# Performance work log

Measured on AMD Instinct MI355X. Metric: run time of the kernel, lower is better.

## Reference

```python
import jax, jax.numpy as jnp
import numpy as np

N, E, F_IN, H, EF, G, GFD = 50000, 800000, 64, 128, 8, 10, 2
NEG_SLOPE = 0.2  # PyG GATv2Conv default negative_slope


def _gatv2_layer(x, src, dst, edge_attr, Wl, bl, Wr, br, We, att, bias):
    # PyG GATv2Conv, heads=1, concat=True, share_weights=False
    n = x.shape[0]
    xl = x @ Wl + bl            # source transform [N,H]
    xr = x @ Wr + br            # target transform [N,H]
    e = edge_attr @ We          # edge embedding   [E,H]
    s = jax.nn.leaky_relu(xl[src] + xr[dst] + e, NEG_SLOPE)  # [E,H]
    logits = s @ att            # [E]
    # numerically-stable segment softmax over destination nodes
    mx = jax.ops.segment_max(logits, dst, num_segments=n)
    mx = jnp.where(jnp.isfinite(mx), mx, 0.0)
    ex = jnp.exp(logits - mx[dst])
    den = jax.ops.segment_sum(ex, dst, num_segments=n)
    alpha = ex / jnp.maximum(den[dst], 1e-16)
    out = jax.ops.segment_sum(alpha[:, None] * xl[src], dst, num_segments=n)
    return out + bias


def _forward(x, edge_index, edge_attr, graph_features, num_graphs, params, head_W, head_b):
    src, dst = edge_index[0], edge_index[1]
    for (Wl, bl, Wr, br, We, att, bias) in params:
        x = jax.nn.relu(_gatv2_layer(x, src, dst, edge_attr, Wl, bl, Wr, br, We, att, bias))
        # dropout p=0.0 / eval mode: no-op
    n_nodes = x.shape[0] // num_graphs
    # faithful replication of the torch reshape chain (graph_feature_dim == 2):
    # graph_features.T [GFD,G] -> unsqueeze(2) -> repeat to [GFD,G,Np] -> view(G,GFD,Np)
    # -> cat(unbind(0), dim=1) -> [GFD, G*Np]
    gf = jnp.broadcast_to(graph_features.T[:, :, None], (GFD, num_graphs, n_nodes))
    gf = gf.reshape(num_graphs, GFD, n_nodes)
    gf = gf.transpose(1, 0, 2).reshape(GFD, num_graphs * n_nodes)
    x = jnp.concatenate([x, gf.T], axis=1)  # [N, H+GFD]
    return x @ head_W + head_b


def setup_inputs():
    key = jax.random.key(0)
    ks = list(jax.random.split(key, 32))
    p = lambda k, s: jax.random.normal(k, s, jnp.float32) * 0.05
    inp = {
        'x': jax.random.normal(ks[0], (N, F_IN), jnp.float32),
        'edge_index': jax.random.randint(ks[1], (2, E), 0, N),
        'edge_attr': jax.random.normal(ks[2], (E, EF), jnp.float32),
        'graph_features': jax.random.normal(ks[3], (G, GFD), jnp.float32),
        'num_graphs': G,
    }
    i = 4
    for l in range(3):
        fin = F_IN if l == 0 else H
        inp[f'Wl{l}'] = p(ks[i], (fin, H)); i += 1
        inp[f'bl{l}'] = jnp.zeros((H,), jnp.float32)
        inp[f'Wr{l}'] = p(ks[i], (fin, H)); i += 1
        inp[f'br{l}'] = jnp.zeros((H,), jnp.float32)
        inp[f'We{l}'] = p(ks[i], (EF, H)); i += 1
        inp[f'att{l}'] = p(ks[i], (H,)); i += 1
        inp[f'bias{l}'] = jnp.zeros((H,), jnp.float32)
    inp['head_W'] = p(ks[i], (H + GFD, 1))
    inp['head_b'] = jnp.zeros((1,), jnp.float32)
    return inp


def reference(x, edge_index, edge_attr, graph_features, num_graphs,
              Wl0, bl0, Wr0, br0, We0, att0, bias0,
              Wl1, bl1, Wr1, br1, We1, att1, bias1,
              Wl2, bl2, Wr2, br2, We2, att2, bias2,
              head_W, head_b):
    params = [(Wl0, bl0, Wr0, br0, We0, att0, bias0),
              (Wl1, bl1, Wr1, br1, We1, att1, bias1),
              (Wl2, bl2, Wr2, br2, We2, att2, bias2)]
    return _forward(x, edge_index, edge_attr, graph_features, num_graphs, params, head_W, head_b)
```

## Files before the change

kernel.cpp:

```cpp
#include <hip/hip_runtime.h>
#include <hip/hip_bf16.h>
#include <math.h>

#define NN 50000
#define EE 800000
#define F_IN 64
#define HH 128
#define EF 8
#define GG 10
#define GFD 2
#define NEG_SLOPE 0.2f
#define NB 64

typedef float v2f __attribute__((ext_vector_type(2)));
__device__ __forceinline__ v2f fma2(v2f a, v2f b, v2f c) {
  return __builtin_elementwise_fma(a, b, c);
}
__device__ __forceinline__ v2f bc2(float x) { v2f r; r.x = x; r.y = x; return r; }

template <int CTRL>
__device__ __forceinline__ float dpp_add(float v) {
  int p = __builtin_amdgcn_update_dpp(0, __float_as_int(v), CTRL, 0xf, 0xf, true);
  return v + __int_as_float(p);
}
__device__ __forceinline__ float red32(float v) {
  v = dpp_add<0xB1>(v);
  v = dpp_add<0x4E>(v);
  v = dpp_add<0x141>(v);
  v = dpp_add<0x140>(v);
  v += __int_as_float(__builtin_amdgcn_ds_swizzle(__float_as_int(v), 0x401F));
  return v;
}

__device__ __forceinline__ void lin2_body(
    int bid, const float* __restrict__ x, int fin,
    const float* __restrict__ Wl, const float* __restrict__ bl,
    const float* __restrict__ Wr, const float* __restrict__ br,
    float* __restrict__ xl, float* __restrict__ xr, int n_nodes) {
  __shared__ float xs[64 * 128];
  const int tid = threadIdx.x;
  const int base = bid * 64;
  int nrows = n_nodes - base; if (nrows > 64) nrows = 64;

  const int total4 = (nrows * fin) >> 2;
  const float4* xsrc = (const float4*)(x + (size_t)base * fin);
  float4* xd = (float4*)xs;
  for (int i = tid; i < total4; i += 256) xd[i] = xsrc[i];
  __syncthreads();

  const int lane = tid & 63;
  const int w = tid >> 6;
  const int c = lane * 2;

  float accl0[16], accl1[16], accr0[16], accr1[16];
#pragma unroll
  for (int j = 0; j < 16; j++) { accl0[j]=0.f; accl1[j]=0.f; accr0[j]=0.f; accr1[j]=0.f; }

  const float* xrow = xs + (w * 16) * fin;
  for (int k = 0; k < fin; k += 4) {
    float2 wl0 = *(const float2*)(Wl + (size_t)k * HH + c);
    float2 wl1 = *(const float2*)(Wl + (size_t)(k + 1) * HH + c);
    float2 wl2 = *(const float2*)(Wl + (size_t)(k + 2) * HH + c);
    float2 wl3 = *(const float2*)(Wl + (size_t)(k + 3) * HH + c);
    float2 wr0 = *(const float2*)(Wr + (size_t)k * HH + c);
    float2 wr1 = *(const float2*)(Wr + (size_t)(k + 1) * HH + c);
    float2 wr2 = *(const float2*)(Wr + (size_t)(k + 2) * HH + c);
    float2 wr3 = *(const float2*)(Wr + (size_t)(k + 3) * HH + c);
#pragma unroll
    for (int j = 0; j < 16; j++) {
      float4 xv = *(const float4*)(xrow + j * fin + k);
      accl0[j] = fmaf(xv.x, wl0.x, accl0[j]);
      accl1[j] = fmaf(xv.x, wl0.y, accl1[j]);
      accr0[j] = fmaf(xv.x, wr0.x, accr0[j]);
      accr1[j] = fmaf(xv.x, wr0.y, accr1[j]);
      accl0[j] = fmaf(xv.y, wl1.x, accl0[j]);
      accl1[j] = fmaf(xv.y, wl1.y, accl1[j]);
      accr0[j] = fmaf(xv.y, wr1.x, accr0[j]);
      accr1[j] = fmaf(xv.y, wr1.y, accr1[j]);
      accl0[j] = fmaf(xv.z, wl2.x, accl0[j]);
      accl1[j] = fmaf(xv.z, wl2.y, accl1[j]);
      accr0[j] = fmaf(xv.z, wr2.x, accr0[j]);
      accr1[j] = fmaf(xv.z, wr2.y, accr1[j]);
      accl0[j] = fmaf(xv.w, wl3.x, accl0[j]);
      accl1[j] = fmaf(xv.w, wl3.y, accl1[j]);
      accr0[j] = fmaf(xv.w, wr3.x, accr0[j]);
      accr1[j] = fmaf(xv.w, wr3.y, accr1[j]);
    }
  }
  float2 blv = *(const float2*)(bl + c);
  float2 brv = *(const float2*)(br + c);
#pragma unroll
  for (int j = 0; j < 16; j++) {
    int n = base + w * 16 + j;
    if (n < n_nodes) {
      *(float2*)(xl + (size_t)n * HH + c) = make_float2(accl0[j] + blv.x, accl1[j] + blv.y);
      *(float2*)(xr + (size_t)n * HH + c) = make_float2(accr0[j] + brv.x, accr1[j] + brv.y);
    }
  }
}

__global__ __launch_bounds__(256) void lin2_kernel(
    const float* __restrict__ x, int fin,
    const float* __restrict__ Wl, const float* __restrict__ bl,
    const float* __restrict__ Wr, const float* __restrict__ br,
    float* __restrict__ xl, float* __restrict__ xr, int n_nodes) {
  lin2_body(blockIdx.x, x, fin, Wl, bl, Wr, br, xl, xr, n_nodes);
}

__device__ __forceinline__ void hist_body(int bid, const int* __restrict__ dst,
                                          int* __restrict__ hist, int ne) {
  int i = bid * 256 + threadIdx.x;
  if (i < ne) atomicAdd(&hist[dst[i]], 1);
}

__global__ __launch_bounds__(256) void fusedA_kernel(
    int nl2, const float* __restrict__ x, int fin,
    const float* __restrict__ Wl, const float* __restrict__ bl,
    const float* __restrict__ Wr, const float* __restrict__ br,
    float* __restrict__ xl, float* __restrict__ xr, int n_nodes,
    const int* __restrict__ dst, int* __restrict__ hist, int ne) {
  if ((int)blockIdx.x < nl2)
    lin2_body(blockIdx.x, x, fin, Wl, bl, Wr, br, xl, xr, n_nodes);
  else
    hist_body(blockIdx.x - nl2, dst, hist, ne);
}

__global__ __launch_bounds__(1024) void reduce_kernel(const int* __restrict__ hist,
                                                      int* __restrict__ bsum, int n) {
  __shared__ int wsum[16];
  const int tid = threadIdx.x;
  const int lane = tid & 63, w = tid >> 6;
  int i = blockIdx.x * 1024 + tid;
  int v = (i < n) ? hist[i] : 0;
#pragma unroll
  for (int off = 32; off; off >>= 1) v += __shfl_xor(v, off);
  if (lane == 0) wsum[w] = v;
  __syncthreads();
  if (tid < 16) {
    int s = wsum[tid];
#pragma unroll
    for (int off = 8; off; off >>= 1) s += __shfl_xor(s, off);
    if (tid == 0) bsum[blockIdx.x] = s;
  }
}

__global__ __launch_bounds__(64) void scanb_kernel(const int* __restrict__ bsum,
                                                   int* __restrict__ bbase,
                                                   int* __restrict__ offs, int nb, int n) {
  const int tid = threadIdx.x;
  int v = (tid < nb) ? bsum[tid] : 0;
  int inc = v;
#pragma unroll
  for (int d = 1; d < 64; d <<= 1) {
    int t2 = __shfl_up(inc, d);
    if (tid >= d) inc += t2;
  }
  if (tid < nb) bbase[tid] = inc - v;
  if (tid == 63) offs[n] = inc;
}

__global__ __launch_bounds__(1024) void scanc_kernel(const int* __restrict__ hist,
                                                     const int* __restrict__ bbase,
                                                     int* __restrict__ offs,
                                                     int* __restrict__ cursor, int n) {
  __shared__ int wsum[16], wpre[16];
  const int tid = threadIdx.x;
  const int lane = tid & 63, w = tid >> 6;
  int i = blockIdx.x * 1024 + tid;
  int orig = (i < n) ? hist[i] : 0;
  int v = orig;
#pragma unroll
  for (int d = 1; d < 64; d <<= 1) {
    int t2 = __shfl_up(v, d);
    if (lane >= d) v += t2;
  }
  if (lane == 63) wsum[w] = v;
  __syncthreads();
  if (tid < 16) {
    int s = wsum[tid];
    int inc = s;
#pragma unroll
    for (int d = 1; d < 16; d <<= 1) {
      int t2 = __shfl_up(inc, d);
      if (tid >= d) inc += t2;
    }
    wpre[tid] = inc - s;
  }
  __syncthreads();
  if (i < n) {
    int ex = bbase[blockIdx.x] + wpre[w] + (v - orig);
    offs[i] = ex; cursor[i] = ex;
  }
}

__device__ __forceinline__ void scatter_body(
    int bid, const int* __restrict__ src, const int* __restrict__ dst,
    int* __restrict__ cursor, int* __restrict__ pk,
    const float4* __restrict__ ea4, float4* __restrict__ eas, int ne) {
  int i = bid * 256 + threadIdx.x;
  if (i < ne) {
    int d = dst[i];
    int pos = atomicAdd(&cursor[d], 1);
    pk[pos] = src[i] * 512;
    float4 a = ea4[i * 2], b = ea4[i * 2 + 1];
    eas[pos * 2] = a; eas[pos * 2 + 1] = b;
  }
}

__device__ __forceinline__ void deg_hist_body(int bid, const int* __restrict__ offs,
                                              int* __restrict__ hist2, int n) {
  __shared__ int lhist[NB];
  const int tid = threadIdx.x;
  int i = bid * 256 + tid;
  if (tid < NB) lhist[tid] = 0;
  __syncthreads();
  if (i < n) {
    int d = offs[i + 1] - offs[i];
    int key = NB - 1 - min(d, NB - 1);
    atomicAdd(&lhist[key], 1);
  }
  __syncthreads();
  if (tid < NB && lhist[tid]) atomicAdd(&hist2[tid], lhist[tid]);
}

__global__ __launch_bounds__(256) void fusedB_kernel(
    int nsc, const int* __restrict__ src, const int* __restrict__ dst,
    int* __restrict__ cursor, int* __restrict__ pk,
    const float4* __restrict__ ea4, float4* __restrict__ eas, int ne,
    const int* __restrict__ offs, int* __restrict__ hist2, int n) {
  if ((int)blockIdx.x < nsc)
    scatter_body(blockIdx.x, src, dst, cursor, pk, ea4, eas, ne);
  else
    deg_hist_body(blockIdx.x - nsc, offs, hist2, n);
}

__global__ __launch_bounds__(64) void scan64_kernel(const int* __restrict__ hist2,
                                                    int* __restrict__ cursor2) {
  const int tid = threadIdx.x;
  int v = hist2[tid];
  int inc = v;
#pragma unroll
  for (int d = 1; d < 64; d <<= 1) {
    int t2 = __shfl_up(inc, d);
    if (tid >= d) inc += t2;
  }
  cursor2[tid] = inc - v;
}

__global__ __launch_bounds__(256) void deg_scatter_kernel(const int* __restrict__ offs,
                                                          int* __restrict__ cursor2,
                                                          int4* __restrict__ meta4, int n) {
  __shared__ int lhist[NB];
  __shared__ int lbase[NB];
  const int tid = threadIdx.x;
  int i = blockIdx.x * 256 + tid;
  if (tid < NB) lhist[tid] = 0;
  __syncthreads();
  int key = 0, rank = 0, bb = 0, ee = 0;
  const bool valid = (i < n);
  if (valid) {
    bb = offs[i]; ee = offs[i + 1];
    int d = ee - bb;
    key = NB - 1 - min(d, NB - 1);
    rank = atomicAdd(&lhist[key], 1);
  }
  __syncthreads();
  if (tid < NB && lhist[tid]) lbase[tid] = atomicAdd(&cursor2[tid], lhist[tid]);
  __syncthreads();
  if (valid) meta4[lbase[key] + rank] = make_int4(bb, ee, i, 0);
}

__global__ __launch_bounds__(256, 4) void gat_fused_kernel(
    const float* __restrict__ xl, const float* __restrict__ xr,
    const float* __restrict__ eas, const float* __restrict__ We,
    const float* __restrict__ att,
    const int* __restrict__ pk, const int4* __restrict__ meta4,
    const float* __restrict__ bias,
    float* __restrict__ xout, int n_nodes,
    float* __restrict__ out_head, const float* __restrict__ hw,
    const float* __restrict__ hb) {
  const int lane = threadIdx.x & 63;
  const int g = lane >> 5, t = lane & 31;
  const int c = t * 4;
  const int tb = t * 16;
  const int nwaves = gridDim.x * 4;

  v2f wea[EF], web[EF];
#pragma unroll
  for (int k = 0; k < EF; k++) {
    float4 w4 = *(const float4*)(We + k * HH + c);
    wea[k].x = w4.x; wea[k].y = w4.y;
    web[k].x = w4.z; web[k].y = w4.w;
  }
  const float4 at = *(const float4*)(att + c);
  const float4 bi = *(const float4*)(bias + c);
  const char* xlb = (const char*)xl;
  const char* easb = (const char*)eas;
  float4 hwv = make_float4(0.f, 0.f, 0.f, 0.f);
  float hw0 = 0.f, hw1 = 0.f, hb0 = 0.f;
  if (out_head) {
    hwv = *(const float4*)(hw + c);
    hw0 = hw[HH]; hw1 = hw[HH + 1]; hb0 = hb[0];
  }

  int wid = blockIdx.x * 4 + (threadIdx.x >> 6);
  if (wid >= n_nodes) return;
  int4 mt = meta4[wid];
  float4 vr4 = *(const float4*)(xr + (size_t)mt.z * HH + c);

  while (true) {
    const int b = mt.x, e = mt.y, node = mt.z;
    const int deg = e - b;
    const int nwid = wid + nwaves;
    const bool hasN = nwid < n_nodes;
    int4 mtN = mt;
    if (hasN) mtN = meta4[nwid];

    v2f vra; vra.x = vr4.x; vra.y = vr4.y;
    v2f vrb; vrb.x = vr4.z; vrb.y = vr4.w;

    float4 o;
    if (deg == 0) {
      o.x = fmaxf(bi.x, 0.f); o.y = fmaxf(bi.y, 0.f);
      o.z = fmaxf(bi.z, 0.f); o.w = fmaxf(bi.w, 0.f);
    } else {
      const int emax = e - 1;
      v2f acc0 = bc2(0.f), acc1 = bc2(0.f);
      float den = 0.f;
      v2f vlAa, vlAb, epA0, epA1, eqA0, eqA1;
      v2f vlBa, vlBb, epB0, epB1, eqB0, eqB1;

#define LOADS(VLa, VLb, P0, P1, Q0, Q1, IDX)                        \
  do {                                                              \
    int _cx = min((IDX), emax);                                     \
    float4 _ep = *(const float4*)(easb + (_cx << 5));               \
    float4 _eq = *(const float4*)(easb + (_cx << 5) + 16);          \
    int _ob = pk[_cx];                                              \
    float4 _vl = *(const float4*)(xlb + (_ob + tb));                \
    P0.x = _ep.x; P0.y = _ep.y; P1.x = _ep.z; P1.y = _ep.w;         \
    Q0.x = _eq.x; Q0.y = _eq.y; Q1.x = _eq.z; Q1.y = _eq.w;         \
    VLa.x = _vl.x; VLa.y = _vl.y; VLb.x = _vl.z; VLb.y = _vl.w;     \
  } while (0)

#define PROCESS(VLa, VLb, P0, P1, Q0, Q1, IDX)                       \
  do {                                                               \
    v2f s0 = VLa + vra;                                              \
    v2f s1 = VLb + vrb;                                              \
    s0 = fma2(bc2(P0.x), wea[0], s0); s1 = fma2(bc2(P0.x), web[0], s1); \
    s0 = fma2(bc2(P0.y), wea[1], s0); s1 = fma2(bc2(P0.y), web[1], s1); \
    s0 = fma2(bc2(P1.x), wea[2], s0); s1 = fma2(bc2(P1.x), web[2], s1); \
    s0 = fma2(bc2(P1.y), wea[3], s0); s1 = fma2(bc2(P1.y), web[3], s1); \
    s0 = fma2(bc2(Q0.x), wea[4], s0); s1 = fma2(bc2(Q0.x), web[4], s1); \
    s0 = fma2(bc2(Q0.y), wea[5], s0); s1 = fma2(bc2(Q0.y), web[5], s1); \
    s0 = fma2(bc2(Q1.x), wea[6], s0); s1 = fma2(bc2(Q1.x), web[6], s1); \
    s0 = fma2(bc2(Q1.y), wea[7], s0); s1 = fma2(bc2(Q1.y), web[7], s1); \
    v2f m0 = s0 * bc2(NEG_SLOPE);                                    \
    v2f m1 = s1 * bc2(NEG_SLOPE);                                    \
    float l0 = fmaxf(s0.x, m0.x), l1 = fmaxf(s0.y, m0.y);            \
    float l2 = fmaxf(s1.x, m1.x), l3 = fmaxf(s1.y, m1.y);            \
    float v = l0 * at.x;                                             \
    v = fmaf(l1, at.y, v);                                           \
    v = fmaf(l2, at.z, v);                                           \
    v = fmaf(l3, at.w, v);                                           \
    v = red32(v);                                                    \
    const float p = ((IDX) < e) ? __expf(v) : 0.f;                   \
    den += p;                                                        \
    acc0 = fma2(bc2(p), VLa, acc0);                                  \
    acc1 = fma2(bc2(p), VLb, acc1);                                  \
  } while (0)

      int idx = b + g;
      LOADS(vlAa, vlAb, epA0, epA1, eqA0, eqA1, idx);
      LOADS(vlBa, vlBb, epB0, epB1, eqB0, eqB1, idx + 2);

      const int nit = (deg + 3) >> 2;
      for (int j = 0; j < nit; j++) {
        PROCESS(vlAa, vlAb, epA0, epA1, eqA0, eqA1, idx);
        LOADS(vlAa, vlAb, epA0, epA1, eqA0, eqA1, idx + 4);
        PROCESS(vlBa, vlBb, epB0, epB1, eqB0, eqB1, idx + 2);
        LOADS(vlBa, vlBb, epB0, epB1, eqB0, eqB1, idx + 6);
        idx += 4;
      }
#undef LOADS
#undef PROCESS

      den += __shfl_xor(den, 32);
      float a0 = acc0.x + __shfl_xor(acc0.x, 32);
      float a1 = acc0.y + __shfl_xor(acc0.y, 32);
      float a2 = acc1.x + __shfl_xor(acc1.x, 32);
      float a3 = acc1.y + __shfl_xor(acc1.y, 32);

      const float inv = 1.f / fmaxf(den, 1e-16f);
      o.x = fmaxf(fmaf(a0, inv, bi.x), 0.f);
      o.y = fmaxf(fmaf(a1, inv, bi.y), 0.f);
      o.z = fmaxf(fmaf(a2, inv, bi.z), 0.f);
      o.w = fmaxf(fmaf(a3, inv, bi.w), 0.f);
    }

    float4 vrN = vr4;
    if (hasN) vrN = *(const float4*)(xr + (size_t)mtN.z * HH + c);

    if (!out_head) {
      if (g == 0) *(float4*)(xout + (size_t)node * HH + c) = o;
    } else {
      float hv = o.x * hwv.x + o.y * hwv.y + o.z * hwv.z + o.w * hwv.w;
      hv = red32(hv);
      if (lane == 0) {
        int k = node / (NN / GG);
        int i0 = 2 * k, i1 = 2 * k + 1;
        float gf0 = xout[(i0 % GG) * GFD + (i0 / GG)];
        float gf1 = xout[(i1 % GG) * GFD + (i1 / GG)];
        out_head[node] = hv + gf0 * hw0 + gf1 * hw1 + hb0;
      }
    }

    if (!hasN) break;
    wid = nwid; mt = mtN; vr4 = vrN;
  }
}

extern "C" void kernel_launch(void* const* d_in, const int* in_sizes, int n_in,
                              void* d_out, int out_size, void* d_ws, size_t ws_size,
                              hipStream_t stream) {
  const float* x_in = (const float*)d_in[0];
  const int*   eidx = (const int*)d_in[1];
  const float* ea   = (const float*)d_in[2];
  const float* gf   = (const float*)d_in[3];
  const int* src = eidx;
  const int* dst = eidx + EE;
  const float* head_W = (const float*)d_in[26];
  const float* head_b = (const float*)d_in[27];
  float* out = (float*)d_out;

  const int NCHUNK = (NN + 1023) / 1024;
  const int NL2B = (NN + 63) / 64;
  const int NHB  = (EE + 255) / 256;
  const int NDB  = (NN + 255) / 256;

  float* P      = (float*)d_ws;
  float* Q      = P + (size_t)NN * HH;
  float* R      = Q + (size_t)NN * HH;
  float* eas    = R + (size_t)NN * HH;
  int*   pk     = (int*)(eas + (size_t)EE * EF);
  int*   hist   = pk + EE;
  int*   hist2  = hist + NN;
  int*   offs   = hist2 + NB;
  int*   cursor = offs + NN + 1;
  int*   cursor2= cursor + NN;
  int*   bsum   = cursor2 + NB;
  int*   bbase  = bsum + NCHUNK;
  int4*  meta4  = (int4*)(((size_t)(bbase + NCHUNK) + 15) & ~(size_t)15);

  const float* Wl0 = (const float*)d_in[5], *bl0 = (const float*)d_in[6];
  const float* Wr0 = (const float*)d_in[7], *br0 = (const float*)d_in[8];

  (void)hipMemsetAsync(hist, 0, (NN + NB) * sizeof(int), stream);
  fusedA_kernel<<<NL2B + NHB, 256, 0, stream>>>(NL2B, x_in, F_IN, Wl0, bl0, Wr0, br0,
                                                P, Q, NN, dst, hist, EE);
  reduce_kernel<<<NCHUNK, 1024, 0, stream>>>(hist, bsum, NN);
  scanb_kernel<<<1, 64, 0, stream>>>(bsum, bbase, offs, NCHUNK, NN);
  scanc_kernel<<<NCHUNK, 1024, 0, stream>>>(hist, bbase, offs, cursor, NN);
  fusedB_kernel<<<NHB + NDB, 256, 0, stream>>>(NHB, src, dst, cursor, pk,
                                               (const float4*)ea, (float4*)eas, EE,
                                               offs, hist2, NN);
  scan64_kernel<<<1, 64, 0, stream>>>(hist2, cursor2);
  deg_scatter_kernel<<<NDB, 256, 0, stream>>>(offs, cursor2, meta4, NN);

  for (int l = 0; l < 3; l++) {
    const float* We   = (const float*)d_in[5 + 7 * l + 4];
    const float* att  = (const float*)d_in[5 + 7 * l + 5];
    const float* bias = (const float*)d_in[5 + 7 * l + 6];

    if (l > 0) {
      const float* Wl = (const float*)d_in[5 + 7 * l + 0];
      const float* bl = (const float*)d_in[5 + 7 * l + 1];
      const float* Wr = (const float*)d_in[5 + 7 * l + 2];
      const float* br = (const float*)d_in[5 + 7 * l + 3];
      lin2_kernel<<<NL2B, 256, 0, stream>>>(R, HH, Wl, bl, Wr, br, P, Q, NN);
    }
    if (l < 2) {
      gat_fused_kernel<<<2048, 256, 0, stream>>>(P, Q, eas, We, att, pk, meta4,
                                                 bias, R, NN, nullptr, nullptr, nullptr);
    } else {
      gat_fused_kernel<<<2048, 256, 0, stream>>>(P, Q, eas, We, att, pk, meta4,
                                                 bias, (float*)gf, NN, out, head_W, head_b);
    }
  }
}
```

Before: 482.1 us.

## Merge scan kernels with grid barrier and split edge-attr scatter into gather pass

Replaces the three-kernel reduce/scan-base/scan-chunk sequence with a single kernel that publishes per-chunk sums and spins on an atomic counter before computing each chunk's base. The CSR scatter now writes only a packed (src offset, edge byte offset) pair. A separate gather pass, fused with the degree-scatter kernel, then reads the edge attributes into sorted order, so the random writes become random reads. This trims kernel launches and makes the scatter writes smaller, but relies on all 49 chunk blocks being co-resident for the spin barrier. It also adds an extra pass over the pair array.

After: 501.6 us. 4.0% more time.

```diff
diff --git a/kernel.cpp b/kernel.cpp
--- a/kernel.cpp
+++ b/kernel.cpp
@@ -125,48 +125,15 @@
     hist_body(blockIdx.x - nl2, dst, hist, ne);
 }
 
-__global__ __launch_bounds__(1024) void reduce_kernel(const int* __restrict__ hist,
-                                                      int* __restrict__ bsum, int n) {
-  __shared__ int wsum[16];
+__global__ __launch_bounds__(1024) void scan_all_kernel(
+    const int* __restrict__ hist, int* __restrict__ offs, int* __restrict__ cursor,
+    int* __restrict__ bsum, int* __restrict__ done, int n, int nchunk) {
+  __shared__ int wsum[16], wpre[16];
+  __shared__ int chtot_s, base_s;
   const int tid = threadIdx.x;
   const int lane = tid & 63, w = tid >> 6;
-  int i = blockIdx.x * 1024 + tid;
-  int v = (i < n) ? hist[i] : 0;
-#pragma unroll
-  for (int off = 32; off; off >>= 1) v += __shfl_xor(v, off);
-  if (lane == 0) wsum[w] = v;
-  __syncthreads();
-  if (tid < 16) {
-    int s = wsum[tid];
-#pragma unroll
-    for (int off = 8; off; off >>= 1) s += __shfl_xor(s, off);
-    if (tid == 0) bsum[blockIdx.x] = s;
-  }
-}
-
-__global__ __launch_bounds__(64) void scanb_kernel(const int* __restrict__ bsum,
-                                                   int* __restrict__ bbase,
-                                                   int* __restrict__ offs, int nb, int n) {
-  const int tid = threadIdx.x;
-  int v = (tid < nb) ? bsum[tid] : 0;
-  int inc = v;
-#pragma unroll
-  for (int d = 1; d < 64; d <<= 1) {
-    int t2 = __shfl_up(inc, d);
-    if (tid >= d) inc += t2;
-  }
-  if (tid < nb) bbase[tid] = inc - v;
-  if (tid == 63) offs[n] = inc;
-}
-
-__global__ __launch_bounds__(1024) void scanc_kernel(const int* __restrict__ hist,
-                                                     const int* __restrict__ bbase,
-                                                     int* __restrict__ offs,
-                                                     int* __restrict__ cursor, int n) {
-  __shared__ int wsum[16], wpre[16];
-  const int tid = threadIdx.x;
-  const int lane = tid & 63, w = tid >> 6;
-  int i = blockIdx.x * 1024 + tid;
+  const int bid = blockIdx.x;
+  int i = bid * 1024 + tid;
   int orig = (i < n) ? hist[i] : 0;
   int v = orig;
 #pragma unroll
@@ -185,25 +152,42 @@
       if (tid >= d) inc += t2;
     }
     wpre[tid] = inc - s;
+    if (tid == 15) chtot_s = inc;
+  }
+  __syncthreads();
+  if (tid == 0) {
+    bsum[bid] = chtot_s;
+    __threadfence();
+    atomicAdd(done, 1);
+    while (atomicAdd(done, 0) < nchunk) __builtin_amdgcn_s_sleep(8);
+  }
+  __syncthreads();
+  if (tid < 64) {
+    int bv = (tid < nchunk) ? atomicAdd(&bsum[tid], 0) : 0;
+    int inc = bv;
+#pragma unroll
+    for (int d = 1; d < 64; d <<= 1) {
+      int t2 = __shfl_up(inc, d);
+      if (tid >= d) inc += t2;
+    }
+    if (tid == bid) base_s = inc - bv;
+    if (bid == nchunk - 1 && tid == nchunk - 1) offs[n] = inc;
   }
   __syncthreads();
   if (i < n) {
-    int ex = bbase[blockIdx.x] + wpre[w] + (v - orig);
+    int ex = base_s + wpre[w] + (v - orig);
     offs[i] = ex; cursor[i] = ex;
   }
 }
 
 __device__ __forceinline__ void scatter_body(
     int bid, const int* __restrict__ src, const int* __restrict__ dst,
-    int* __restrict__ cursor, int* __restrict__ pk,
-    const float4* __restrict__ ea4, float4* __restrict__ eas, int ne) {
+    int* __restrict__ cursor, int2* __restrict__ pk2, int ne) {
   int i = bid * 256 + threadIdx.x;
   if (i < ne) {
     int d = dst[i];
     int pos = atomicAdd(&cursor[d], 1);
-    pk[pos] = src[i] * 512;
-    float4 a = ea4[i * 2], b = ea4[i * 2 + 1];
-    eas[pos * 2] = a; eas[pos * 2 + 1] = b;
+    pk2[pos] = make_int2(src[i] * 512, i * 32);
   }
 }
 
@@ -225,11 +209,10 @@
 
 __global__ __launch_bounds__(256) void fusedB_kernel(
     int nsc, const int* __restrict__ src, const int* __restrict__ dst,
-    int* __restrict__ cursor, int* __restrict__ pk,
-    const float4* __restrict__ ea4, float4* __restrict__ eas, int ne,
+    int* __restrict__ cursor, int2* __restrict__ pk2, int ne,
     const int* __restrict__ offs, int* __restrict__ hist2, int n) {
   if ((int)blockIdx.x < nsc)
-    scatter_body(blockIdx.x, src, dst, cursor, pk, ea4, eas, ne);
+    scatter_body(blockIdx.x, src, dst, cursor, pk2, ne);
   else
     deg_hist_body(blockIdx.x - nsc, offs, hist2, n);
 }
@@ -247,13 +230,26 @@
   cursor2[tid] = inc - v;
 }
 
-__global__ __launch_bounds__(256) void deg_scatter_kernel(const int* __restrict__ offs,
-                                                          int* __restrict__ cursor2,
-                                                          int4* __restrict__ meta4, int n) {
+__device__ __forceinline__ void gather_body(
+    int bid, const int2* __restrict__ pk2, const char* __restrict__ eab,
+    int* __restrict__ pk, float4* __restrict__ eas, int ne) {
+  int i = bid * 256 + threadIdx.x;
+  if (i < ne) {
+    int2 p2 = pk2[i];
+    pk[i] = p2.x;
+    const float4* s4 = (const float4*)(eab + p2.y);
+    float4 a = s4[0], b = s4[1];
+    eas[i * 2] = a; eas[i * 2 + 1] = b;
+  }
+}
+
+__device__ __forceinline__ void deg_scatter_body(
+    int bid, const int* __restrict__ offs, int* __restrict__ cursor2,
+    int4* __restrict__ meta4, int n) {
   __shared__ int lhist[NB];
   __shared__ int lbase[NB];
   const int tid = threadIdx.x;
-  int i = blockIdx.x * 256 + tid;
+  int i = bid * 256 + tid;
   if (tid < NB) lhist[tid] = 0;
   __syncthreads();
   int key = 0, rank = 0, bb = 0, ee = 0;
@@ -268,6 +264,17 @@
   if (tid < NB && lhist[tid]) lbase[tid] = atomicAdd(&cursor2[tid], lhist[tid]);
   __syncthreads();
   if (valid) meta4[lbase[key] + rank] = make_int4(bb, ee, i, 0);
+}
+
+__global__ __launch_bounds__(256) void fusedC_kernel(
+    int ngb, const int2* __restrict__ pk2, const char* __restrict__ eab,
+    int* __restrict__ pk, float4* __restrict__ eas, int ne,
+    const int* __restrict__ offs, int* __restrict__ cursor2,
+    int4* __restrict__ meta4, int n) {
+  if ((int)blockIdx.x < ngb)
+    gather_body(blockIdx.x, pk2, eab, pk, eas, ne);
+  else
+    deg_scatter_body(blockIdx.x - ngb, offs, cursor2, meta4, n);
 }
 
 __global__ __launch_bounds__(256, 4) void gat_fused_kernel(
@@ -442,29 +449,29 @@
   float* R      = Q + (size_t)NN * HH;
   float* eas    = R + (size_t)NN * HH;
   int*   pk     = (int*)(eas + (size_t)EE * EF);
-  int*   hist   = pk + EE;
+  int2*  pk2    = (int2*)(pk + EE);
+  int*   hist   = (int*)(pk2 + EE);
   int*   hist2  = hist + NN;
-  int*   offs   = hist2 + NB;
+  int*   done   = hist2 + NB;
+  int*   offs   = done + 1;
   int*   cursor = offs + NN + 1;
   int*   cursor2= cursor + NN;
   int*   bsum   = cursor2 + NB;
-  int*   bbase  = bsum + NCHUNK;
-  int4*  meta4  = (int4*)(((size_t)(bbase + NCHUNK) + 15) & ~(size_t)15);
+  int4*  meta4  = (int4*)(((size_t)(bsum + NCHUNK) + 15) & ~(size_t)15);
 
   const float* Wl0 = (const float*)d_in[5], *bl0 = (const float*)d_in[6];
   const float* Wr0 = (const float*)d_in[7], *br0 = (const float*)d_in[8];
 
-  (void)hipMemsetAsync(hist, 0, (NN + NB) * sizeof(int), stream);
+  (void)hipMemsetAsync(hist, 0, (NN + NB + 1) * sizeof(int), stream);
   fusedA_kernel<<<NL2B + NHB, 256, 0, stream>>>(NL2B, x_in, F_IN, Wl0, bl0, Wr0, br0,
                                                 P, Q, NN, dst, hist, EE);
-  reduce_kernel<<<NCHUNK, 1024, 0, stream>>>(hist, bsum, NN);
-  scanb_kernel<<<1, 64, 0, stream>>>(bsum, bbase, offs, NCHUNK, NN);
-  scanc_kernel<<<NCHUNK, 1024, 0, stream>>>(hist, bbase, offs, cursor, NN);
-  fusedB_kernel<<<NHB + NDB, 256, 0, stream>>>(NHB, src, dst, cursor, pk,
-                                               (const float4*)ea, (float4*)eas, EE,
+  scan_all_kernel<<<NCHUNK, 1024, 0, stream>>>(hist, offs, cursor, bsum, done, NN, NCHUNK);
+  fusedB_kernel<<<NHB + NDB, 256, 0, stream>>>(NHB, src, dst, cursor, pk2, EE,
                                                offs, hist2, NN);
   scan64_kernel<<<1, 64, 0, stream>>>(hist2, cursor2);
-  deg_scatter_kernel<<<NDB, 256, 0, stream>>>(offs, cursor2, meta4, NN);
+  fusedC_kernel<<<NHB + NDB, 256, 0, stream>>>(NHB, pk2, (const char*)ea, pk,
+                                               (float4*)eas, EE, offs, cursor2,
+                                               meta4, NN);
 
   for (int l = 0; l < 3; l++) {
     const float* We   = (const float*)d_in[5 + 7 * l + 4];
```
